# Performance work log

Measured on AMD Instinct MI355X. Metric: run time of the kernel, lower is better.

## Reference

```python
import jax, jax.numpy as jnp
import numpy as np
from jax import lax

D_MODEL = 1024
N_EXPERTS = 8
N_ACTIVE = 2
FFN_HIDDEN = int(D_MODEL * 2.0)


def setup_inputs() -> dict:
    key = jax.random.key(0)
    ks = jax.random.split(key, 7)
    B, T = 2, 2048
    s_in = 1.0 / np.sqrt(D_MODEL)
    s_h = 1.0 / np.sqrt(FFN_HIDDEN)
    return {
        "x": jax.random.normal(ks[0], (B, T, D_MODEL), dtype=jnp.float32),
        # router: torch Linear(d_model, n_experts, bias=False) weight [E, D]
        "router_w": jax.random.uniform(ks[1], (N_EXPERTS, D_MODEL), jnp.float32, -s_in, s_in),
        # stacked expert FFN params: w1 [E, H, D], b1 [E, H], w2 [E, D, H], b2 [E, D]
        "w1": jax.random.uniform(ks[2], (N_EXPERTS, FFN_HIDDEN, D_MODEL), jnp.float32, -s_in, s_in),
        "b1": jax.random.uniform(ks[3], (N_EXPERTS, FFN_HIDDEN), jnp.float32, -s_in, s_in),
        "w2": jax.random.uniform(ks[4], (N_EXPERTS, D_MODEL, FFN_HIDDEN), jnp.float32, -s_h, s_h),
        "b2": jax.random.uniform(ks[5], (N_EXPERTS, D_MODEL), jnp.float32, -s_h, s_h),
    }


def reference(x, router_w, w1, b1, w2, b2):
    B, T, D = x.shape
    N = B * T
    xf = x.reshape(N, D)

    logits = xf @ router_w.T                      # [N, E]
    probs = jax.nn.softmax(logits, axis=-1)       # [N, E]

    # --- aux load-balancing loss (f_i is non-differentiable, from indices) ---
    _, disp_idx = lax.top_k(logits, N_ACTIVE)     # [N, K]
    disp_mask = jax.nn.one_hot(disp_idx, N_EXPERTS, dtype=logits.dtype).sum(axis=1)  # [N, E]
    f_i = disp_mask.sum(axis=0) / (N * N_ACTIVE)  # [E]
    P_i = probs.mean(axis=0)                      # [E]
    aux_loss = N_EXPERTS * jnp.sum(f_i * P_i)

    # --- top-k combine weights, renormalized ---
    topk_w, topk_idx = lax.top_k(probs, N_ACTIVE)                 # [N, K]
    topk_w = topk_w / topk_w.sum(axis=-1, keepdims=True)
    # scatter top-k weights into dense [N, E] combine matrix (zeros elsewhere)
    combine_w = (jax.nn.one_hot(topk_idx, N_EXPERTS, dtype=xf.dtype) * topk_w[..., None]).sum(axis=1)

    # --- expert FFNs, weighted combine (loop over small fixed expert set) ---
    out = jnp.zeros_like(xf)
    for e in range(N_EXPERTS):
        h = jax.nn.silu(xf @ w1[e].T + b1[e])     # [N, H]
        y = h @ w2[e].T + b2[e]                   # [N, D]
        out = out + combine_w[:, e:e + 1] * y

    return out.reshape(B, T, D), aux_loss
```

## Files before the change

### kernel.cpp

```cpp
#include <hip/hip_runtime.h>
#include <cstdint>
#include <cstddef>

#define D_MODEL 1024
#define N_EXPERTS 8
#define FFN_H 2048
#define N_TOK 4096
#define CAP 2048

typedef float f32x4 __attribute__((ext_vector_type(4)));
typedef __bf16 bf16x8 __attribute__((ext_vector_type(8)));

static constexpr size_t XB_OFF   = 0;
static constexpr size_t W1B_OFF  = XB_OFF  + (size_t)N_TOK * D_MODEL * 2;
static constexpr size_t W2B_OFF  = W1B_OFF + (size_t)N_EXPERTS * FFN_H * D_MODEL * 2;
static constexpr size_t HBUF_OFF = W2B_OFF + (size_t)N_EXPERTS * D_MODEL * FFN_H * 2;
static constexpr size_t YBUF_OFF = HBUF_OFF + (size_t)N_EXPERTS * CAP * FFN_H * 2;
static constexpr size_t CNT_OFF  = YBUF_OFF + (size_t)N_EXPERTS * CAP * D_MODEL * 2;
static constexpr size_t PSUM_OFF = CNT_OFF + 32;
static constexpr size_t TOK_OFF  = PSUM_OFF + 32;
static constexpr size_t TIX_OFF  = TOK_OFF + (size_t)N_EXPERTS * CAP * 4;
static constexpr size_t TIW_OFF  = TIX_OFF + (size_t)N_TOK * 8;

__device__ __forceinline__ void async_ld16(const void* g, void* l) {
    __builtin_amdgcn_global_load_lds(
        (const __attribute__((address_space(1))) unsigned int*)g,
        (__attribute__((address_space(3))) unsigned int*)l, 16, 0, 0);
}

__device__ __forceinline__ void cvt_block(const float* __restrict__ src,
                                          __bf16* __restrict__ dst,
                                          int c, int tid) {
    size_t i = (size_t)c * 2048 + (size_t)tid * 8;
    float4 a = *reinterpret_cast<const float4*>(src + i);
    float4 d = *reinterpret_cast<const float4*>(src + i + 4);
    bf16x8 r;
    r[0] = (__bf16)a.x; r[1] = (__bf16)a.y; r[2] = (__bf16)a.z; r[3] = (__bf16)a.w;
    r[4] = (__bf16)d.x; r[5] = (__bf16)d.y; r[6] = (__bf16)d.z; r[7] = (__bf16)d.w;
    *reinterpret_cast<bf16x8*>(dst + i) = r;
}

__global__ __launch_bounds__(256) void prep_kernel(const float* __restrict__ x,
                                                   const float* __restrict__ rw,
                                                   const float* __restrict__ w1,
                                                   __bf16* __restrict__ xb,
                                                   __bf16* __restrict__ w1b,
                                                   int* __restrict__ counts,
                                                   float* __restrict__ psum,
                                                   int* __restrict__ tok_list,
                                                   int2* __restrict__ tinfo_idx,
                                                   float2* __restrict__ tinfo_w) {
    __shared__ float rws[N_EXPERTS * D_MODEL];
    __shared__ int s_e0[64], s_e1[64], s_r0[64], s_r1[64];
    __shared__ float s_w0[64], s_w1[64];
    __shared__ int hist[8], base[8];
    __shared__ float pacc[8];

    int tid = threadIdx.x;
    int b = blockIdx.x;
    if (b >= 64) {
        int c = b - 64;
        if (c < 2048) cvt_block(x, xb, c, tid);
        else          cvt_block(w1, w1b, c - 2048, tid);
        return;
    }

    for (int i = tid * 4; i < N_EXPERTS * D_MODEL; i += 256 * 4)
        *reinterpret_cast<float4*>(&rws[i]) = *reinterpret_cast<const float4*>(&rw[i]);
    if (tid < 8) { hist[tid] = 0; pacc[tid] = 0.f; }
    __syncthreads();

    int wave = tid >> 6, lane = tid & 63;
    float psacc[8] = {};
    for (int it = 0; it < 16; ++it) {
        int li = wave * 16 + it;
        int t = b * 64 + li;
        const float* xr = x + (size_t)t * D_MODEL;
        float acc[8] = {};
#pragma unroll
        for (int i = 0; i < D_MODEL / 64; ++i) {
            float xv = xr[lane + 64 * i];
#pragma unroll
            for (int e = 0; e < 8; ++e) acc[e] += xv * rws[e * D_MODEL + lane + 64 * i];
        }
        float logit[8];
#pragma unroll
        for (int e = 0; e < 8; ++e) {
            float v = acc[e];
            for (int off = 32; off; off >>= 1) v += __shfl_xor(v, off);
            logit[e] = v;
        }
        float mx = logit[0];
#pragma unroll
        for (int e = 1; e < 8; ++e) mx = fmaxf(mx, logit[e]);
        float p[8], s = 0.f;
#pragma unroll
        for (int e = 0; e < 8; ++e) { p[e] = expf(logit[e] - mx); s += p[e]; }
        float inv = 1.f / s;
#pragma unroll
        for (int e = 0; e < 8; ++e) { p[e] *= inv; psacc[e] += p[e]; }
        int e0 = 0; float p0 = p[0];
#pragma unroll
        for (int e = 1; e < 8; ++e) if (p[e] > p0) { p0 = p[e]; e0 = e; }
        int e1 = -1; float p1 = -1.f;
#pragma unroll
        for (int e = 0; e < 8; ++e) if (e != e0 && p[e] > p1) { p1 = p[e]; e1 = e; }
        float invw = 1.f / (p0 + p1);
        if (lane == 0) {
            s_e0[li] = e0; s_e1[li] = e1;
            s_w0[li] = p0 * invw; s_w1[li] = p1 * invw;
        }
    }
    if (lane == 0)
#pragma unroll
        for (int e = 0; e < 8; ++e) atomicAdd(&pacc[e], psacc[e]);
    __syncthreads();

    if (tid < 64) {
        s_r0[tid] = atomicAdd(&hist[s_e0[tid]], 1);
        s_r1[tid] = atomicAdd(&hist[s_e1[tid]], 1);
    }
    __syncthreads();
    if (tid < 8) {
        base[tid] = atomicAdd(&counts[tid], hist[tid]);
        atomicAdd(&psum[tid], pacc[tid]);
    }
    __syncthreads();
    if (tid < 64) {
        int t = b * 64 + tid;
        int e0 = s_e0[tid], e1 = s_e1[tid];
        int q0 = min(base[e0] + s_r0[tid], CAP - 1);
        int q1 = min(base[e1] + s_r1[tid], CAP - 1);
        tok_list[e0 * CAP + q0] = t;
        tok_list[e1 * CAP + q1] = t;
        tinfo_idx[t] = make_int2(e0 * CAP + q0, e1 * CAP + q1);
        tinfo_w[t] = make_float2(s_w0[tid], s_w1[tid]);
    }
}

template <int KDIM, bool PASS2, bool CVT>
__global__ __launch_bounds__(256, 2) void ffn_kernel(const __bf16* __restrict__ A_base,
                                                     const __bf16* __restrict__ B_base,
                                                     const float* __restrict__ bias,
                                                     const int* __restrict__ counts,
                                                     const int* __restrict__ tok_list,
                                                     __bf16* __restrict__ Out_base,
                                                     const float* __restrict__ cvt_src,
                                                     __bf16* __restrict__ cvt_dst,
                                                     int ngemm) {
    constexpr int BROWS = PASS2 ? D_MODEL : FFN_H;
    constexpr int NT = BROWS / 128;
    constexpr int NSTEP = KDIM / 64;
    int bid = blockIdx.x;
    int tid = threadIdx.x;

    if (CVT && bid >= ngemm) {
        cvt_block(cvt_src, cvt_dst, bid - ngemm, tid);
        return;
    }

    int e = bid & 7;
    int r = bid >> 3;
    int n0 = (r % NT) * 128;
    int m0 = (r / NT) * 128;
    int cnt = min(counts[e], CAP);
    if (m0 >= cnt) return;

    __shared__ char smem[65536];

    int* s_tok = (int*)smem;
    if (!PASS2 && tid < 128) {
        int slot = min(m0 + tid, cnt - 1);
        s_tok[tid] = tok_list[e * CAP + slot];
    }
    __syncthreads();

    int colk = ((tid & 3) ^ ((tid >> 3) & 3)) * 8;
    const __bf16 *a_src0, *a_src1;
    if (PASS2) {
        int s0 = min(m0 + (tid >> 2), cnt - 1);
        int s1 = min(m0 + 64 + (tid >> 2), cnt - 1);
        a_src0 = A_base + ((size_t)e * CAP + s0) * KDIM + colk;
        a_src1 = A_base + ((size_t)e * CAP + s1) * KDIM + colk;
    } else {
        a_src0 = A_base + (size_t)s_tok[tid >> 2] * KDIM + colk;
        a_src1 = A_base + (size_t)s_tok[64 + (tid >> 2)] * KDIM + colk;
    }
    const __bf16* b_src0 = B_base + ((size_t)e * BROWS + n0 + (tid >> 2)) * KDIM + colk;
    const __bf16* b_src1 = b_src0 + (size_t)64 * KDIM;
    __syncthreads();

    int wv = tid >> 6, lane = tid & 63;
    int wm = wv >> 1, wn = wv & 1;
    int lm = lane & 15, q = lane >> 4;
    int rsw = (q ^ ((lm >> 1) & 3)) * 8;
    int a_base = (wm * 64 + lm) * 32 + rsw;
    int b_base = (wn * 64 + lm) * 32 + rsw;

    char* wofs_a = smem + (tid >> 6) * 1024;
    char* wofs_b = smem + 32768 + (tid >> 6) * 1024;

    f32x4 acc[4][4] = {};

    {
        char* la = wofs_a; char* lb = wofs_b;
        async_ld16(a_src0,      la);        async_ld16(a_src1,      la + 4096);
        async_ld16(a_src0 + 32, la + 8192); async_ld16(a_src1 + 32, la + 8192 + 4096);
        async_ld16(b_src0,      lb);        async_ld16(b_src1,      lb + 4096);
        async_ld16(b_src0 + 32, lb + 8192); async_ld16(b_src1 + 32, lb + 8192 + 4096);
    }
    __syncthreads();

    int cur = 0;
    for (int t = 0; t < NSTEP; ++t) {
        if (t + 1 < NSTEP) {
            int k0 = (t + 1) * 64;
            char* la = wofs_a + ((cur ^ 1) * 16384);
            char* lb = wofs_b + ((cur ^ 1) * 16384);
            async_ld16(a_src0 + k0,      la);        async_ld16(a_src1 + k0,      la + 4096);
            async_ld16(a_src0 + k0 + 32, la + 8192); async_ld16(a_src1 + k0 + 32, la + 8192 + 4096);
            async_ld16(b_src0 + k0,      lb);        async_ld16(b_src1 + k0,      lb + 4096);
            async_ld16(b_src0 + k0 + 32, lb + 8192); async_ld16(b_src1 + k0 + 32, lb + 8192 + 4096);
        }
#pragma unroll
        for (int kk = 0; kk < 2; ++kk) {
            const __bf16* pa = (const __bf16*)(smem + (cur * 2 + kk) * 8192);
            const __bf16* pb = (const __bf16*)(smem + 32768 + (cur * 2 + kk) * 8192);
            bf16x8 af[4], bfg[4];
#pragma unroll
            for (int f = 0; f < 4; ++f) {
                af[f]  = *reinterpret_cast<const bf16x8*>(&pa[a_base + f * 512]);
                bfg[f] = *reinterpret_cast<const bf16x8*>(&pb[b_base + f * 512]);
            }
#pragma unroll
            for (int fm = 0; fm < 4; ++fm)
#pragma unroll
                for (int fn = 0; fn < 4; ++fn)
                    acc[fm][fn] = __builtin_amdgcn_mfma_f32_16x16x32_bf16(af[fm], bfg[fn], acc[fm][fn], 0, 0, 0);
        }
        __syncthreads();
        cur ^= 1;
    }

    __bf16* ep = (__bf16*)(smem) + wv * (64 * 72);
#pragma unroll
    for (int fn = 0; fn < 4; ++fn) {
        int n = n0 + wn * 64 + fn * 16 + lm;
        float bv = bias[e * BROWS + n];
#pragma unroll
        for (int fm = 0; fm < 4; ++fm)
#pragma unroll
            for (int i = 0; i < 4; ++i) {
                float v = acc[fm][fn][i] + bv;
                if (!PASS2) v = v / (1.f + __expf(-v));
                ep[(fm * 16 + q * 4 + i) * 72 + fn * 16 + lm] = (__bf16)v;
            }
    }
    __syncthreads();
    int rr = lane >> 3, ccol = (lane & 7) * 8;
#pragma unroll
    for (int rep = 0; rep < 8; ++rep) {
        int rw = rep * 8 + rr;
        int slot = m0 + wm * 64 + rw;
        bf16x8 vv = *reinterpret_cast<const bf16x8*>(&ep[rw * 72 + ccol]);
        if (slot < cnt)
            *reinterpret_cast<bf16x8*>(
                &Out_base[((size_t)e * CAP + slot) * BROWS + n0 + wn * 64 + ccol]) = vv;
    }
}

__global__ __launch_bounds__(256) void combine_kernel(const __bf16* __restrict__ ybuf,
                                                      const int2* __restrict__ tinfo_idx,
                                                      const float2* __restrict__ tinfo_w,
                                                      const int* __restrict__ counts,
                                                      const float* __restrict__ psum,
                                                      float* __restrict__ out) {
    int tid = threadIdx.x;
    if (blockIdx.x == 0 && tid == 0) {
        float s = 0.f;
#pragma unroll
        for (int e = 0; e < 8; ++e)
            s += ((float)counts[e] / (float)(N_TOK * 2)) * (psum[e] / (float)N_TOK);
        out[(size_t)N_TOK * D_MODEL] = 8.f * s;
    }
    int t = blockIdx.x * 2 + (tid >> 7);
    int d0 = (tid & 127) * 8;
    int2 ix = tinfo_idx[t];
    float2 w = tinfo_w[t];
    bf16x8 ya = *reinterpret_cast<const bf16x8*>(ybuf + (size_t)ix.x * D_MODEL + d0);
    bf16x8 yb = *reinterpret_cast<const bf16x8*>(ybuf + (size_t)ix.y * D_MODEL + d0);
    float4 o0, o1;
    o0.x = w.x * (float)ya[0] + w.y * (float)yb[0];
    o0.y = w.x * (float)ya[1] + w.y * (float)yb[1];
    o0.z = w.x * (float)ya[2] + w.y * (float)yb[2];
    o0.w = w.x * (float)ya[3] + w.y * (float)yb[3];
    o1.x = w.x * (float)ya[4] + w.y * (float)yb[4];
    o1.y = w.x * (float)ya[5] + w.y * (float)yb[5];
    o1.z = w.x * (float)ya[6] + w.y * (float)yb[6];
    o1.w = w.x * (float)ya[7] + w.y * (float)yb[7];
    float* op = out + (size_t)t * D_MODEL + d0;
    *reinterpret_cast<float4*>(op) = o0;
    *reinterpret_cast<float4*>(op + 4) = o1;
}

extern "C" void kernel_launch(void* const* d_in, const int* in_sizes, int n_in,
                              void* d_out, int out_size, void* d_ws, size_t ws_size,
                              hipStream_t stream) {
    const float* x  = (const float*)d_in[0];
    const float* rw = (const float*)d_in[1];
    const float* w1 = (const float*)d_in[2];
    const float* b1 = (const float*)d_in[3];
    const float* w2 = (const float*)d_in[4];
    const float* b2 = (const float*)d_in[5];
    float* out = (float*)d_out;

    char* ws = (char*)d_ws;
    __bf16* xb     = (__bf16*)(ws + XB_OFF);
    __bf16* w1b    = (__bf16*)(ws + W1B_OFF);
    __bf16* w2b    = (__bf16*)(ws + W2B_OFF);
    __bf16* hbuf   = (__bf16*)(ws + HBUF_OFF);
    __bf16* ybuf   = (__bf16*)(ws + YBUF_OFF);
    int*    counts = (int*)(ws + CNT_OFF);
    float*  psum   = (float*)(ws + PSUM_OFF);
    int*    tok    = (int*)(ws + TOK_OFF);
    int2*   tix    = (int2*)(ws + TIX_OFF);
    float2* tiw    = (float2*)(ws + TIW_OFF);

    hipMemsetAsync(ws + CNT_OFF, 0, 64, stream);

    prep_kernel<<<64 + 2048 + 8192, 256, 0, stream>>>(x, rw, w1, xb, w1b,
                                                      counts, psum, tok, tix, tiw);

    constexpr int NG1 = 8 * (FFN_H / 128) * (CAP / 128);
    ffn_kernel<D_MODEL, false, true><<<NG1 + 8192, 256, 0, stream>>>(
        xb, w1b, b1, counts, tok, hbuf, w2, w2b, NG1);

    constexpr int NG2 = 8 * (D_MODEL / 128) * (CAP / 128);
    ffn_kernel<FFN_H, true, false><<<NG2, 256, 0, stream>>>(
        hbuf, w2b, b2, counts, tok, ybuf, nullptr, nullptr, NG2);

    combine_kernel<<<N_TOK / 2, 256, 0, stream>>>(ybuf, tix, tiw, counts, psum, out);
}
```

Baseline: 284.5 us.

## Halve K-step to shrink LDS, raise occupancy, interleave convert blocks with GEMM tiles

The GEMM main loop now stages 32-wide K slices instead of 64-wide. This cuts shared memory per block from 64KB to 36KB and lets launch bounds request 4 blocks per CU instead of 2. The fused weight-convert blocks are now interleaved one GEMM tile per four convert blocks, rather than appended after all GEMM tiles, so conversion bandwidth overlaps with compute. In exchange there are twice as many barriers per K, and register pressure may rise under the tighter launch bound.

```diff
diff --git a/kernel.cpp b/kernel.cpp
--- a/kernel.cpp
+++ b/kernel.cpp
@@ -139,34 +139,40 @@
 }
 
 template <int KDIM, bool PASS2, bool CVT>
-__global__ __launch_bounds__(256, 2) void ffn_kernel(const __bf16* __restrict__ A_base,
+__global__ __launch_bounds__(256, 4) void ffn_kernel(const __bf16* __restrict__ A_base,
                                                      const __bf16* __restrict__ B_base,
                                                      const float* __restrict__ bias,
                                                      const int* __restrict__ counts,
                                                      const int* __restrict__ tok_list,
                                                      __bf16* __restrict__ Out_base,
                                                      const float* __restrict__ cvt_src,
-                                                     __bf16* __restrict__ cvt_dst,
-                                                     int ngemm) {
+                                                     __bf16* __restrict__ cvt_dst) {
     constexpr int BROWS = PASS2 ? D_MODEL : FFN_H;
     constexpr int NT = BROWS / 128;
-    constexpr int NSTEP = KDIM / 64;
+    constexpr int NSTEP = KDIM / 32;
     int bid = blockIdx.x;
     int tid = threadIdx.x;
 
-    if (CVT && bid >= ngemm) {
-        cvt_block(cvt_src, cvt_dst, bid - ngemm, tid);
-        return;
-    }
-
-    int e = bid & 7;
-    int r = bid >> 3;
+    int gid;
+    if (CVT) {
+        int m5 = bid % 5;
+        if (m5) {
+            cvt_block(cvt_src, cvt_dst, (bid / 5) * 4 + m5 - 1, tid);
+            return;
+        }
+        gid = bid / 5;
+    } else {
+        gid = bid;
+    }
+
+    int e = gid & 7;
+    int r = gid >> 3;
     int n0 = (r % NT) * 128;
     int m0 = (r / NT) * 128;
     int cnt = min(counts[e], CAP);
     if (m0 >= cnt) return;
 
-    __shared__ char smem[65536];
+    __shared__ char smem[36864];
 
     int* s_tok = (int*)smem;
     if (!PASS2 && tid < 128) {
@@ -196,50 +202,43 @@
     int rsw = (q ^ ((lm >> 1) & 3)) * 8;
     int a_base = (wm * 64 + lm) * 32 + rsw;
     int b_base = (wn * 64 + lm) * 32 + rsw;
-
-    char* wofs_a = smem + (tid >> 6) * 1024;
-    char* wofs_b = smem + 32768 + (tid >> 6) * 1024;
+    int wofs = wv * 1024;
 
     f32x4 acc[4][4] = {};
 
-    {
-        char* la = wofs_a; char* lb = wofs_b;
-        async_ld16(a_src0,      la);        async_ld16(a_src1,      la + 4096);
-        async_ld16(a_src0 + 32, la + 8192); async_ld16(a_src1 + 32, la + 8192 + 4096);
-        async_ld16(b_src0,      lb);        async_ld16(b_src1,      lb + 4096);
-        async_ld16(b_src0 + 32, lb + 8192); async_ld16(b_src1 + 32, lb + 8192 + 4096);
-    }
-    __syncthreads();
-
-    int cur = 0;
+    auto stage = [&](int t) {
+        int k0 = t * 32;
+        int bo = (t & 1) * 8192;
+        char* la = smem + bo + wofs;
+        char* lb = smem + 16384 + bo + wofs;
+        async_ld16(a_src0 + k0, la);
+        async_ld16(a_src1 + k0, la + 4096);
+        async_ld16(b_src0 + k0, lb);
+        async_ld16(b_src1 + k0, lb + 4096);
+    };
+    auto compute = [&](int t) {
+        int bo = (t & 1) * 8192;
+        const __bf16* pa = (const __bf16*)(smem + bo);
+        const __bf16* pb = (const __bf16*)(smem + 16384 + bo);
+        bf16x8 af[4], bfg[4];
+#pragma unroll
+        for (int f = 0; f < 4; ++f) {
+            af[f]  = *reinterpret_cast<const bf16x8*>(&pa[a_base + f * 512]);
+            bfg[f] = *reinterpret_cast<const bf16x8*>(&pb[b_base + f * 512]);
+        }
+#pragma unroll
+        for (int fm = 0; fm < 4; ++fm)
+#pragma unroll
+            for (int fn = 0; fn < 4; ++fn)
+                acc[fm][fn] = __builtin_amdgcn_mfma_f32_16x16x32_bf16(af[fm], bfg[fn], acc[fm][fn], 0, 0, 0);
+    };
+
+    stage(0);
+    __syncthreads();
     for (int t = 0; t < NSTEP; ++t) {
-        if (t + 1 < NSTEP) {
-            int k0 = (t + 1) * 64;
-            char* la = wofs_a + ((cur ^ 1) * 16384);
-            char* lb = wofs_b + ((cur ^ 1) * 16384);
-            async_ld16(a_src0 + k0,      la);        async_ld16(a_src1 + k0,      la + 4096);
-            async_ld16(a_src0 + k0 + 32, la + 8192); async_ld16(a_src1 + k0 + 32, la + 8192 + 4096);
-            async_ld16(b_src0 + k0,      lb);        async_ld16(b_src1 + k0,      lb + 4096);
-            async_ld16(b_src0 + k0 + 32, lb + 8192); async_ld16(b_src1 + k0 + 32, lb + 8192 + 4096);
-        }
-#pragma unroll
-        for (int kk = 0; kk < 2; ++kk) {
-            const __bf16* pa = (const __bf16*)(smem + (cur * 2 + kk) * 8192);
-            const __bf16* pb = (const __bf16*)(smem + 32768 + (cur * 2 + kk) * 8192);
-            bf16x8 af[4], bfg[4];
-#pragma unroll
-            for (int f = 0; f < 4; ++f) {
-                af[f]  = *reinterpret_cast<const bf16x8*>(&pa[a_base + f * 512]);
-                bfg[f] = *reinterpret_cast<const bf16x8*>(&pb[b_base + f * 512]);
-            }
-#pragma unroll
-            for (int fm = 0; fm < 4; ++fm)
-#pragma unroll
-                for (int fn = 0; fn < 4; ++fn)
-                    acc[fm][fn] = __builtin_amdgcn_mfma_f32_16x16x32_bf16(af[fm], bfg[fn], acc[fm][fn], 0, 0, 0);
-        }
+        if (t + 1 < NSTEP) stage(t + 1);
+        compute(t);
         __syncthreads();
-        cur ^= 1;
     }
 
     __bf16* ep = (__bf16*)(smem) + wv * (64 * 72);
@@ -333,11 +332,11 @@
 
     constexpr int NG1 = 8 * (FFN_H / 128) * (CAP / 128);
     ffn_kernel<D_MODEL, false, true><<<NG1 + 8192, 256, 0, stream>>>(
-        xb, w1b, b1, counts, tok, hbuf, w2, w2b, NG1);
+        xb, w1b, b1, counts, tok, hbuf, w2, w2b);
 
     constexpr int NG2 = 8 * (D_MODEL / 128) * (CAP / 128);
     ffn_kernel<FFN_H, true, false><<<NG2, 256, 0, stream>>>(
-        hbuf, w2b, b2, counts, tok, ybuf, nullptr, nullptr, NG2);
+        hbuf, w2b, b2, counts, tok, ybuf, nullptr, nullptr);
 
     combine_kernel<<<N_TOK / 2, 256, 0, stream>>>(ybuf, tix, tiw, counts, psum, out);
 }
```

Result: no change. 283.9 us (-0.2%).
